# Kernel optimization log

Measured on AMD Instinct MI355X. Metric: run time of the kernel, lower is better.

## Reference

```python
import jax, jax.numpy as jnp
import numpy as np

T, N, D, H, E = 12, 10000, 256, 512, 160000
NUM_CONVS = 2  # num_layers - 1


def setup_inputs() -> dict:
    key = jax.random.key(0)
    ks = jax.random.split(key, 12)
    s_in = 1.0 / np.sqrt(D)
    s_h = 1.0 / np.sqrt(H)
    return {
        "xs": jax.random.normal(ks[0], (T, N, D), dtype=jnp.float32),
        "edge_index": jax.random.randint(ks[1], (2, E), 0, N, dtype=jnp.int64),
        "edge_weight": jax.random.uniform(ks[2], (E,), dtype=jnp.float32),
        # GRUCell params (PyTorch layout: [3H, D], [3H, H], [3H], [3H])
        "W_ih": jax.random.normal(ks[3], (3 * H, D), dtype=jnp.float32) * s_in,
        "W_hh": jax.random.normal(ks[4], (3 * H, H), dtype=jnp.float32) * s_h,
        "b_ih": jax.random.normal(ks[5], (3 * H,), dtype=jnp.float32) * s_h,
        "b_hh": jax.random.normal(ks[6], (3 * H,), dtype=jnp.float32) * s_h,
        # stacked GCNConv params
        "conv_W": jax.random.normal(ks[7], (NUM_CONVS, H, H), dtype=jnp.float32) * s_h,
        "conv_b": jnp.zeros((NUM_CONVS, H), dtype=jnp.float32),
        # final Linear(hidden_dim, 1)
        "lin_W": jax.random.normal(ks[8], (H, 1), dtype=jnp.float32) * s_h,
        "lin_b": jnp.zeros((1,), dtype=jnp.float32),
    }


def gru_cell(x, h, W_ih, W_hh, b_ih, b_hh):
    gi = x @ W_ih.T + b_ih  # (N, 3H)
    gh = h @ W_hh.T + b_hh  # (N, 3H)
    i_r, i_z, i_n = jnp.split(gi, 3, axis=-1)
    h_r, h_z, h_n = jnp.split(gh, 3, axis=-1)
    r = jax.nn.sigmoid(i_r + h_r)
    z = jax.nn.sigmoid(i_z + h_z)
    n = jnp.tanh(i_n + r * h_n)
    return (1.0 - z) * n + z * h


def reference(xs, edge_index, edge_weight, W_ih, W_hh, b_ih, b_hh,
              conv_W, conv_b, lin_W, lin_b):
    row, col = edge_index[0], edge_index[1]
    # GCN symmetric normalization with self-loops (PyG GCNConv default)
    deg = jax.ops.segment_sum(edge_weight, col, num_segments=N) + 1.0
    dinv = jax.lax.rsqrt(deg)
    norm = dinv[row] * edge_weight * dinv[col]  # (E,)
    self_w = dinv * dinv                        # (N,) self-loop coefficient

    def gcn(h, W, b):
        hW = h @ W  # (N, H)
        msg = norm[:, None] * hW[row]           # gather + weight
        agg = jax.ops.segment_sum(msg, col, num_segments=N)  # scatter-add
        return agg + self_w[:, None] * hW + b

    def step(h, x):
        h = gru_cell(x, h, W_ih, W_hh, b_ih, b_hh)
        for l in range(NUM_CONVS):
            h = jax.nn.relu(gcn(h, conv_W[l], conv_b[l]))
        # dropout is identity in eval mode
        out = h @ lin_W + lin_b  # (N, 1)
        return h, out

    h0 = jnp.zeros((N, H), dtype=xs.dtype)
    _, outs = jax.lax.scan(step, h0, xs)
    return outs  # (T, N, 1)
```

## Files before the change

kernel.cpp:

```cpp
#include <hip/hip_runtime.h>
#include <math.h>

#define T_STEPS 12
#define N_NODES 10000
#define MP 10112
#define D_IN 256
#define H_DIM 512
#define H3 1536
#define E_EDGES 160000
#define NUM_CONVS 2

typedef _Float16 f16x8 __attribute__((ext_vector_type(8)));
typedef float floatx4 __attribute__((ext_vector_type(4)));
typedef _Float16 f16x4 __attribute__((ext_vector_type(4)));
typedef unsigned short u16;
typedef unsigned int u32;

__device__ __forceinline__ float sigmoid_f(float x) {
  return __builtin_amdgcn_rcpf(1.0f + __expf(-x));
}
__device__ __forceinline__ float tanh_f(float x) {
  return 1.0f - 2.0f * __builtin_amdgcn_rcpf(1.0f + __expf(2.0f * x));
}

__device__ __forceinline__ void glds16(const void* g, void* l) {
  __builtin_amdgcn_global_load_lds(
      (const __attribute__((address_space(1))) unsigned int*)g,
      (__attribute__((address_space(3))) unsigned int*)l, 16, 0, 0);
}

#define MFMA16H(a, b, c) __builtin_amdgcn_mfma_f32_16x16x32_f16((a), (b), (c), 0, 0, 0)

__global__ __launch_bounds__(256) void gru_fused(
    const _Float16* __restrict__ X16,
    const _Float16* __restrict__ S16,
    const _Float16* __restrict__ Wih,
    const _Float16* __restrict__ Whh,
    const float* __restrict__ bihg, const float* __restrict__ bhhg,
    _Float16* __restrict__ G16) {
  __shared__ _Float16 As[4096];
  __shared__ _Float16 Bs[3072];
  const int tid = threadIdx.x;
  const int lane = tid & 63;
  const int wave = tid >> 6;
  const int bid = blockIdx.y * 16 + blockIdx.x;
  const int lid = (bid & 7) * 158 + (bid >> 3);
  const int bx = lid & 15, by = lid >> 4;
  const int rbase = by * 128;
  const int cbase = bx * 96;

  const int sa1 = tid, sa2 = tid + 256;
  const int ra1 = sa1 >> 2, ca1 = (sa1 & 3) ^ ((ra1 >> 1) & 3);
  const int ra2 = sa2 >> 2, ca2 = (sa2 & 3) ^ ((ra2 >> 1) & 3);
  const int la1 = (sa1 >> 6) << 9;
  const int la2 = (sa2 >> 6) << 9;
  const int sb1 = tid;
  const int rb1 = sb1 >> 2, cb1 = (sb1 & 3) ^ ((rb1 >> 1) & 3);
  const int lb1 = (sb1 >> 6) << 9;
  const int sb2 = 256 + tid;
  const int rb2 = sb2 >> 2, cb2 = (sb2 & 3) ^ ((rb2 >> 1) & 3);
  const int lb2 = (sb2 >> 6) << 9;

  const int wr = (wave >> 1) * 64;
  const int wc = (wave & 1) * 48;
  const int lrow = lane & 15;
  const int kq = lane >> 4;
  const int swz = kq ^ ((lrow >> 1) & 3);
  const int aoff = (wr + lrow) * 32 + swz * 8;
  const int boff = (wc + lrow) * 32 + swz * 8;

  floatx4 acc[4][4];
#pragma unroll
  for (int i = 0; i < 4; ++i)
#pragma unroll
    for (int g = 0; g < 4; ++g) acc[i][g] = (floatx4){0.f, 0.f, 0.f, 0.f};

  {
    const _Float16* pa1 = X16 + (size_t)(rbase + ra1) * 256 + ca1 * 8;
    const _Float16* pa2 = X16 + (size_t)(rbase + ra2) * 256 + ca2 * 8;
    const _Float16* pb1 = Wih + (size_t)(cbase + rb1) * 256 + cb1 * 8;
    const _Float16* pb2 = Wih + (size_t)(cbase + rb2) * 256 + cb2 * 8;
    for (int kt = 0; kt < 256; kt += 32) {
      glds16(pa1 + kt, &As[la1]);
      glds16(pa2 + kt, &As[la2]);
      glds16(pb1 + kt, &Bs[lb1]);
      if (tid < 128) glds16(pb2 + kt, &Bs[lb2]);
      __syncthreads();
      f16x8 ah[4], bh[3];
#pragma unroll
      for (int i = 0; i < 4; ++i) ah[i] = *(const f16x8*)&As[aoff + i * 512];
#pragma unroll
      for (int g = 0; g < 3; ++g) bh[g] = *(const f16x8*)&Bs[boff + g * 512];
#pragma unroll
      for (int i = 0; i < 4; ++i) {
        acc[i][0] = MFMA16H(ah[i], bh[0], acc[i][0]);
        acc[i][1] = MFMA16H(ah[i], bh[1], acc[i][1]);
        acc[i][2] = MFMA16H(ah[i], bh[2], acc[i][2]);
      }
      __syncthreads();
    }
  }
  {
    const _Float16* pa1 = S16 + (size_t)(rbase + ra1) * 512 + ca1 * 8;
    const _Float16* pa2 = S16 + (size_t)(rbase + ra2) * 512 + ca2 * 8;
    const _Float16* pb1 = Whh + (size_t)(cbase + rb1) * 512 + cb1 * 8;
    const _Float16* pb2 = Whh + (size_t)(cbase + rb2) * 512 + cb2 * 8;
    for (int kt = 0; kt < 512; kt += 32) {
      glds16(pa1 + kt, &As[la1]);
      glds16(pa2 + kt, &As[la2]);
      glds16(pb1 + kt, &Bs[lb1]);
      if (tid < 128) glds16(pb2 + kt, &Bs[lb2]);
      __syncthreads();
      f16x8 ah[4], bh[3];
#pragma unroll
      for (int i = 0; i < 4; ++i) ah[i] = *(const f16x8*)&As[aoff + i * 512];
#pragma unroll
      for (int g = 0; g < 3; ++g) bh[g] = *(const f16x8*)&Bs[boff + g * 512];
#pragma unroll
      for (int i = 0; i < 4; ++i) {
        acc[i][0] = MFMA16H(ah[i], bh[0], acc[i][0]);
        acc[i][1] = MFMA16H(ah[i], bh[1], acc[i][1]);
        acc[i][3] = MFMA16H(ah[i], bh[2], acc[i][3]);
      }
      __syncthreads();
    }
  }

  const int c0g = cbase + wc + lrow;
  const int j = (((bx << 1) | (wave & 1)) << 4) | lrow;
  const float brz0 = bihg[c0g] + bhhg[c0g];
  const float brz1 = bihg[c0g + 16] + bhhg[c0g + 16];
  const float bin = bihg[c0g + 32];
  const float bhn = bhhg[c0g + 32];
#pragma unroll
  for (int i = 0; i < 4; ++i) {
    int r0 = rbase + wr + i * 16 + kq * 4;
#pragma unroll
    for (int rr = 0; rr < 4; ++rr) {
      int row = r0 + rr;
      if (row >= N_NODES) continue;
      float r = sigmoid_f(acc[i][0][rr] + brz0);
      float z = sigmoid_f(acc[i][1][rr] + brz1);
      float nn = tanh_f(acc[i][2][rr] + bin + r * (acc[i][3][rr] + bhn));
      size_t o = (size_t)row * H_DIM + j;
      float hp = (float)S16[o];
      float hv = (1.0f - z) * nn + z * hp;
      G16[o] = (_Float16)hv;
    }
  }
}

__global__ __launch_bounds__(256) void gemm_conv(
    const u16* __restrict__ A16, const u16* __restrict__ B16,
    _Float16* __restrict__ C, int M, int Nn, int K) {
  __shared__ u16 As[2][2048];
  __shared__ u16 Bs[2][4096];
  const int tid = threadIdx.x;
  const int lane = tid & 63;
  const int wave = tid >> 6;
  const int bid = blockIdx.y * 4 + blockIdx.x;
  const int lid = (bid & 7) * 79 + (bid >> 3);
  const int bx = lid & 3, by = lid >> 2;
  const int rbase = by * 64;
  const int cbase = bx * 128;

  const int sa = tid;
  const int ra = sa >> 2, ca = (sa & 3) ^ ((ra >> 1) & 3);
  const int la = (sa >> 6) << 9;
  const int sb1 = tid, sb2 = tid + 256;
  const int rb1 = sb1 >> 2, cb1 = (sb1 & 3) ^ ((rb1 >> 1) & 3);
  const int rb2 = sb2 >> 2, cb2 = (sb2 & 3) ^ ((rb2 >> 1) & 3);
  const int lb1 = (sb1 >> 6) << 9, lb2 = (sb2 >> 6) << 9;
  const size_t oA = (size_t)(rbase + ra) * K + ca * 8;
  const size_t oB1 = (size_t)(cbase + rb1) * K + cb1 * 8;
  const size_t oB2 = (size_t)(cbase + rb2) * K + cb2 * 8;

  const int wr = (wave >> 1) * 32;
  const int wc = (wave & 1) * 64;
  const int lrow = lane & 15;
  const int kq = lane >> 4;
  const int swz = kq ^ ((lrow >> 1) & 3);
  const int aoff = (wr + lrow) * 32 + swz * 8;
  const int boff = (wc + lrow) * 32 + swz * 8;

  auto stage = [&](int buf, int t) {
    const int kt = t * 32;
    glds16(A16 + oA + kt, &As[buf][la]);
    glds16(B16 + oB1 + kt, &Bs[buf][lb1]);
    glds16(B16 + oB2 + kt, &Bs[buf][lb2]);
  };

  floatx4 acc[2][4];
#pragma unroll
  for (int i = 0; i < 2; ++i)
#pragma unroll
    for (int jj = 0; jj < 4; ++jj) acc[i][jj] = (floatx4){0.f, 0.f, 0.f, 0.f};

  const int NT = K >> 5;
  stage(0, 0);
  stage(1, 1);
  int cur = 0;
  for (int t = 0; t < NT; ++t) {
    if (t < NT - 1) asm volatile("s_waitcnt vmcnt(3)" ::: "memory");
    else            asm volatile("s_waitcnt vmcnt(0)" ::: "memory");
    __builtin_amdgcn_s_barrier();
    __builtin_amdgcn_sched_barrier(0);
    {
      f16x8 ah[2], bh[4];
#pragma unroll
      for (int i = 0; i < 2; ++i) ah[i] = *(const f16x8*)&As[cur][aoff + i * 512];
#pragma unroll
      for (int jj = 0; jj < 4; ++jj) bh[jj] = *(const f16x8*)&Bs[cur][boff + jj * 512];
      __builtin_amdgcn_s_setprio(1);
#pragma unroll
      for (int i = 0; i < 2; ++i)
#pragma unroll
        for (int jj = 0; jj < 4; ++jj) acc[i][jj] = MFMA16H(ah[i], bh[jj], acc[i][jj]);
      __builtin_amdgcn_s_setprio(0);
      __builtin_amdgcn_s_barrier();
    }
    __builtin_amdgcn_sched_barrier(0);
    if (t + 2 < NT) stage(cur, t + 2);
    cur ^= 1;
  }

#pragma unroll
  for (int jj = 0; jj < 4; ++jj) {
    int col = cbase + wc + jj * 16 + lrow;
#pragma unroll
    for (int i = 0; i < 2; ++i) {
      int r0 = rbase + wr + i * 16 + kq * 4;
#pragma unroll
      for (int rr = 0; rr < 4; ++rr) {
        int row = r0 + rr;
        if (row < M) C[(size_t)row * Nn + col] = (_Float16)acc[i][jj][rr];
      }
    }
  }
}

__global__ void split_grouped16(const float* __restrict__ W, _Float16* __restrict__ w16,
                                int K) {
  int i = blockIdx.x * 256 + threadIdx.x;
  if (i >= H3 * K) return;
  int r3h = i / K, k = i - r3h * K;
  int g = r3h >> 9, j = r3h & 511;
  int nr = ((j >> 4) * 48) + (g << 4) + (j & 15);
  w16[(size_t)nr * K + k] = (_Float16)W[i];
}

__global__ void bias_grouped(const float* __restrict__ bih, const float* __restrict__ bhh,
                             float* __restrict__ bihg, float* __restrict__ bhhg) {
  int n = blockIdx.x * 256 + threadIdx.x;
  if (n >= H3) return;
  int g = n >> 9, j = n & 511;
  int nr = ((j >> 4) * 48) + (g << 4) + (j & 15);
  bihg[nr] = bih[n];
  bhhg[nr] = bhh[n];
}

__global__ void split_convw(const float* __restrict__ W, _Float16* __restrict__ w16) {
  int o = blockIdx.x * 256 + threadIdx.x;
  if (o >= NUM_CONVS * H_DIM * H_DIM) return;
  int k = o & 511, j = (o >> 9) & 511, l = o >> 18;
  float v = W[(size_t)l * H_DIM * H_DIM + (size_t)k * H_DIM + j];
  w16[o] = (_Float16)v;
}

__global__ void split_xs16(const float* __restrict__ xs, _Float16* __restrict__ x16) {
  const int QP = MP * D_IN / 4;
  int q = blockIdx.x * 256 + threadIdx.x;
  if (q >= T_STEPS * QP) return;
  int t = q / QP;
  int rem = (q - t * QP) * 4;
  size_t o = (size_t)t * MP * D_IN + rem;
  f16x4 v16 = {(_Float16)0.f, (_Float16)0.f, (_Float16)0.f, (_Float16)0.f};
  if (rem < N_NODES * D_IN) {
    float4 v = *(const float4*)(xs + (size_t)t * N_NODES * D_IN + rem);
    v16[0] = (_Float16)v.x;
    v16[1] = (_Float16)v.y;
    v16[2] = (_Float16)v.z;
    v16[3] = (_Float16)v.w;
  }
  *(f16x4*)(x16 + o) = v16;
}

__global__ void deg_kernel(const int* __restrict__ col, const float* __restrict__ w,
                           float* __restrict__ deg, int* __restrict__ counts) {
  int e = blockIdx.x * blockDim.x + threadIdx.x;
  if (e >= E_EDGES) return;
  int c = col[e];
  atomicAdd(&deg[c], w[e]);
  atomicAdd(&counts[c], 1);
}

__global__ void dinv_kernel(float* __restrict__ deg_dinv, float* __restrict__ selfw) {
  int n = blockIdx.x * blockDim.x + threadIdx.x;
  if (n >= N_NODES) return;
  float d = deg_dinv[n] + 1.0f;
  float di = 1.0f / sqrtf(d);
  deg_dinv[n] = di;
  selfw[n] = 1.0f / d;
}

__global__ __launch_bounds__(1024) void scan_kernel(const int* __restrict__ counts,
                                                    int* __restrict__ offsets, int n) {
  __shared__ int smem[1024];
  __shared__ int carry_s;
  if (threadIdx.x == 0) carry_s = 0;
  __syncthreads();
  for (int base = 0; base < n; base += 1024) {
    int i = base + threadIdx.x;
    int v = (i < n) ? counts[i] : 0;
    smem[threadIdx.x] = v;
    __syncthreads();
    for (int off = 1; off < 1024; off <<= 1) {
      int t = (threadIdx.x >= off) ? smem[threadIdx.x - off] : 0;
      __syncthreads();
      smem[threadIdx.x] += t;
      __syncthreads();
    }
    if (i < n) offsets[i] = carry_s + smem[threadIdx.x] - v;
    int total = smem[1023];
    __syncthreads();
    if (threadIdx.x == 0) carry_s += total;
    __syncthreads();
  }
  if (threadIdx.x == 0) offsets[n] = carry_s;
}

__global__ void scatter_kernel(const int* __restrict__ row, const int* __restrict__ col,
                               const float* __restrict__ w, const float* __restrict__ dinv,
                               const int* __restrict__ offsets, int* __restrict__ cursor,
                               int* __restrict__ csr_row, float* __restrict__ csr_norm) {
  int e = blockIdx.x * blockDim.x + threadIdx.x;
  if (e >= E_EDGES) return;
  int r = row[e], c = col[e];
  float nrm = dinv[r] * w[e] * dinv[c];
  int pos = offsets[c] + atomicAdd(&cursor[c], 1);
  csr_row[pos] = r;
  csr_norm[pos] = nrm;
}

__device__ __forceinline__ void fma8h(float* a, float w, const _Float16* p) {
  f16x4 x = *(const f16x4*)p;
  f16x4 y = *(const f16x4*)(p + 256);
  a[0] = fmaf(w, (float)x[0], a[0]);
  a[1] = fmaf(w, (float)x[1], a[1]);
  a[2] = fmaf(w, (float)x[2], a[2]);
  a[3] = fmaf(w, (float)x[3], a[3]);
  a[4] = fmaf(w, (float)y[0], a[4]);
  a[5] = fmaf(w, (float)y[1], a[5]);
  a[6] = fmaf(w, (float)y[2], a[6]);
  a[7] = fmaf(w, (float)y[3], a[7]);
}

template <bool FINAL>
__global__ __launch_bounds__(256) void agg_kernel(
    const _Float16* __restrict__ hW, const int* __restrict__ csr_row,
    const float* __restrict__ csr_norm, const int* __restrict__ offsets,
    const float* __restrict__ selfw, const float* __restrict__ bias,
    _Float16* __restrict__ dst,
    const float* __restrict__ lw, const float* __restrict__ lb,
    float* __restrict__ out) {
  const int n = (blockIdx.x << 2) | (threadIdx.x >> 6);
  const int lane = threadIdx.x & 63;
  if (n >= N_NODES) return;
  const int c0 = lane << 2;
  const int beg = offsets[n], end = offsets[n + 1];
  float a0[8] = {}, a1[8] = {};
  int j = beg;
  for (; j + 4 <= end; j += 4) {
    int r0 = csr_row[j], r1 = csr_row[j + 1], r2 = csr_row[j + 2], r3 = csr_row[j + 3];
    float w0 = csr_norm[j], w1 = csr_norm[j + 1], w2 = csr_norm[j + 2], w3 = csr_norm[j + 3];
    fma8h(a0, w0, hW + (size_t)r0 * H_DIM + c0);
    fma8h(a1, w1, hW + (size_t)r1 * H_DIM + c0);
    fma8h(a0, w2, hW + (size_t)r2 * H_DIM + c0);
    fma8h(a1, w3, hW + (size_t)r3 * H_DIM + c0);
  }
  for (; j < end; ++j) fma8h(a0, csr_norm[j], hW + (size_t)csr_row[j] * H_DIM + c0);

  const float sw = selfw[n];
  const _Float16* ps = hW + (size_t)n * H_DIM + c0;
  f16x4 sa = *(const f16x4*)ps;
  f16x4 sb = *(const f16x4*)(ps + 256);
  float4 ba = *(const float4*)(bias + c0);
  float4 bb = *(const float4*)(bias + 256 + c0);
  float v[8];
  v[0] = fmaxf(fmaf(sw, (float)sa[0], a0[0] + a1[0]) + ba.x, 0.f);
  v[1] = fmaxf(fmaf(sw, (float)sa[1], a0[1] + a1[1]) + ba.y, 0.f);
  v[2] = fmaxf(fmaf(sw, (float)sa[2], a0[2] + a1[2]) + ba.z, 0.f);
  v[3] = fmaxf(fmaf(sw, (float)sa[3], a0[3] + a1[3]) + ba.w, 0.f);
  v[4] = fmaxf(fmaf(sw, (float)sb[0], a0[4] + a1[4]) + bb.x, 0.f);
  v[5] = fmaxf(fmaf(sw, (float)sb[1], a0[5] + a1[5]) + bb.y, 0.f);
  v[6] = fmaxf(fmaf(sw, (float)sb[2], a0[6] + a1[6]) + bb.z, 0.f);
  v[7] = fmaxf(fmaf(sw, (float)sb[3], a0[7] + a1[7]) + bb.w, 0.f);

  size_t o = (size_t)n * H_DIM + c0;
  f16x4 ga = {(_Float16)v[0], (_Float16)v[1], (_Float16)v[2], (_Float16)v[3]};
  f16x4 gb = {(_Float16)v[4], (_Float16)v[5], (_Float16)v[6], (_Float16)v[7]};
  *(f16x4*)(dst + o) = ga;
  *(f16x4*)(dst + o + 256) = gb;

  if (FINAL) {
    float4 la = *(const float4*)(lw + c0);
    float4 lbv = *(const float4*)(lw + 256 + c0);
    float s = v[0] * la.x + v[1] * la.y + v[2] * la.z + v[3] * la.w +
              v[4] * lbv.x + v[5] * lbv.y + v[6] * lbv.z + v[7] * lbv.w;
#pragma unroll
    for (int off2 = 32; off2 > 0; off2 >>= 1) s += __shfl_down(s, off2, 64);
    if (lane == 0) out[n] = s + lb[0];
  }
}

extern "C" void kernel_launch(void* const* d_in, const int* in_sizes, int n_in,
                              void* d_out, int out_size, void* d_ws, size_t ws_size,
                              hipStream_t stream) {
  const float* xs = (const float*)d_in[0];
  const int* ei = (const int*)d_in[1];
  const float* ew = (const float*)d_in[2];
  const float* W_ih = (const float*)d_in[3];
  const float* W_hh = (const float*)d_in[4];
  const float* b_ih = (const float*)d_in[5];
  const float* b_hh = (const float*)d_in[6];
  const float* conv_W = (const float*)d_in[7];
  const float* conv_b = (const float*)d_in[8];
  const float* lin_W = (const float*)d_in[9];
  const float* lin_b = (const float*)d_in[10];
  float* out = (float*)d_out;

  const int* row = ei;
  const int* col = ei + E_EDGES;

  char* ws = (char*)d_ws;
  size_t off = 0;
  auto alloc = [&](size_t bytes) -> void* {
    void* p = ws + off;
    off += (bytes + 255) & ~(size_t)255;
    return p;
  };
  _Float16* S16 = (_Float16*)alloc((size_t)MP * H_DIM * 2);
  _Float16* G16 = (_Float16*)alloc((size_t)MP * H_DIM * 2);
  _Float16* hW16 = (_Float16*)alloc((size_t)MP * H_DIM * 2);
  _Float16* xs16 = (_Float16*)alloc((size_t)T_STEPS * MP * D_IN * 2);
  _Float16* Wih16 = (_Float16*)alloc((size_t)H3 * D_IN * 2);
  _Float16* Whh16 = (_Float16*)alloc((size_t)H3 * H_DIM * 2);
  _Float16* Wc16 = (_Float16*)alloc((size_t)NUM_CONVS * H_DIM * H_DIM * 2);
  float* bihg = (float*)alloc(H3 * 4);
  float* bhhg = (float*)alloc(H3 * 4);
  float* dinv = (float*)alloc(N_NODES * 4);
  float* selfw = (float*)alloc(N_NODES * 4);
  float* csr_norm = (float*)alloc(E_EDGES * 4);
  int* csr_row = (int*)alloc(E_EDGES * 4);
  int* offsets = (int*)alloc((N_NODES + 1) * 4);
  int* counts = (int*)alloc(N_NODES * 4);
  int* cursor = (int*)alloc(N_NODES * 4);

  hipMemsetAsync(S16, 0, (size_t)MP * H_DIM * 2, stream);
  hipMemsetAsync(G16, 0, (size_t)MP * H_DIM * 2, stream);
  hipMemsetAsync(hW16, 0, (size_t)MP * H_DIM * 2, stream);
  hipMemsetAsync(dinv, 0, N_NODES * 4, stream);
  hipMemsetAsync(counts, 0, N_NODES * 4, stream);
  hipMemsetAsync(cursor, 0, N_NODES * 4, stream);

  deg_kernel<<<(E_EDGES + 255) / 256, 256, 0, stream>>>(col, ew, dinv, counts);
  dinv_kernel<<<(N_NODES + 255) / 256, 256, 0, stream>>>(dinv, selfw);
  scan_kernel<<<1, 1024, 0, stream>>>(counts, offsets, N_NODES);
  scatter_kernel<<<(E_EDGES + 255) / 256, 256, 0, stream>>>(row, col, ew, dinv, offsets,
                                                            cursor, csr_row, csr_norm);
  split_grouped16<<<(H3 * D_IN + 255) / 256, 256, 0, stream>>>(W_ih, Wih16, D_IN);
  split_grouped16<<<(H3 * H_DIM + 255) / 256, 256, 0, stream>>>(W_hh, Whh16, H_DIM);
  bias_grouped<<<(H3 + 255) / 256, 256, 0, stream>>>(b_ih, b_hh, bihg, bhhg);
  split_convw<<<(NUM_CONVS * H_DIM * H_DIM + 255) / 256, 256, 0, stream>>>(conv_W, Wc16);
  split_xs16<<<(T_STEPS * MP * D_IN / 4 + 255) / 256, 256, 0, stream>>>(xs, xs16);

  dim3 blk(256);
  dim3 g_gru(16, MP / 128);
  dim3 g_conv(H_DIM / 128, MP / 64);
  int g_agg = (N_NODES + 3) / 4;

  for (int t = 0; t < T_STEPS; ++t) {
    gru_fused<<<g_gru, blk, 0, stream>>>(
        xs16 + (size_t)t * MP * D_IN, S16, Wih16, Whh16, bihg, bhhg, G16);
    gemm_conv<<<g_conv, blk, 0, stream>>>((const u16*)G16, (const u16*)Wc16, hW16,
                                          N_NODES, H_DIM, H_DIM);
    agg_kernel<false><<<g_agg, 256, 0, stream>>>(
        hW16, csr_row, csr_norm, offsets, selfw, conv_b, G16,
        nullptr, nullptr, nullptr);
    gemm_conv<<<g_conv, blk, 0, stream>>>(
        (const u16*)G16, (const u16*)(Wc16 + (size_t)H_DIM * H_DIM), hW16,
        N_NODES, H_DIM, H_DIM);
    agg_kernel<true><<<g_agg, 256, 0, stream>>>(
        hW16, csr_row, csr_norm, offsets, selfw, conv_b + H_DIM, S16,
        lin_W, lin_b, out + (size_t)t * N_NODES);
  }
}
```

Measured before the change: 1.652 ms.

## Double-buffer GRU GEMM LDS tiles with async prefetch and vmcnt waits

Converts the fused GRU GEMM main loop from single-buffered LDS staging with two syncthreads per k-step into a double-buffered pipeline. The x and hidden-state phases are merged into one 24-step loop that prefetches two stages ahead, waiting with per-wave vmcnt counts (waves 0-1 issue four loads per stage, waves 2-3 three) and raw s_barrier calls. It also raises wave priority around the MFMA bursts. The goal is to hide global-to-LDS load latency behind matrix math, at the cost of doubled LDS use and fragile hand-counted waitcnt logic.

```diff
diff --git a/kernel.cpp b/kernel.cpp
--- a/kernel.cpp
+++ b/kernel.cpp
@@ -31,6 +31,27 @@
 
 #define MFMA16H(a, b, c) __builtin_amdgcn_mfma_f32_16x16x32_f16((a), (b), (c), 0, 0, 0)
 
+template <int G2>
+__device__ __forceinline__ void gru_kstep(const _Float16 (&As)[2][4096],
+                                          const _Float16 (&Bs)[2][3072], int cur,
+                                          int aoff, int boff,
+                                          floatx4 (&acc)[4][4]) {
+  f16x8 ah[4], bh[3];
+#pragma unroll
+  for (int i = 0; i < 4; ++i) ah[i] = *(const f16x8*)&As[cur][aoff + i * 512];
+#pragma unroll
+  for (int g = 0; g < 3; ++g) bh[g] = *(const f16x8*)&Bs[cur][boff + g * 512];
+  __builtin_amdgcn_s_setprio(1);
+#pragma unroll
+  for (int i = 0; i < 4; ++i) {
+    acc[i][0] = MFMA16H(ah[i], bh[0], acc[i][0]);
+    acc[i][1] = MFMA16H(ah[i], bh[1], acc[i][1]);
+    acc[i][G2] = MFMA16H(ah[i], bh[2], acc[i][G2]);
+  }
+  __builtin_amdgcn_s_setprio(0);
+  __builtin_amdgcn_s_barrier();
+}
+
 __global__ __launch_bounds__(256) void gru_fused(
     const _Float16* __restrict__ X16,
     const _Float16* __restrict__ S16,
@@ -38,8 +59,8 @@
     const _Float16* __restrict__ Whh,
     const float* __restrict__ bihg, const float* __restrict__ bhhg,
     _Float16* __restrict__ G16) {
-  __shared__ _Float16 As[4096];
-  __shared__ _Float16 Bs[3072];
+  __shared__ _Float16 As[2][4096];
+  __shared__ _Float16 Bs[2][3072];
   const int tid = threadIdx.x;
   const int lane = tid & 63;
   const int wave = tid >> 6;
@@ -69,61 +90,63 @@
   const int aoff = (wr + lrow) * 32 + swz * 8;
   const int boff = (wc + lrow) * 32 + swz * 8;
 
+  const size_t xA1 = (size_t)(rbase + ra1) * 256 + ca1 * 8;
+  const size_t xA2 = (size_t)(rbase + ra2) * 256 + ca2 * 8;
+  const size_t hA1 = (size_t)(rbase + ra1) * 512 + ca1 * 8;
+  const size_t hA2 = (size_t)(rbase + ra2) * 512 + ca2 * 8;
+  const size_t xB1 = (size_t)(cbase + rb1) * 256 + cb1 * 8;
+  const size_t xB2 = (size_t)(cbase + rb2) * 256 + cb2 * 8;
+  const size_t hB1 = (size_t)(cbase + rb1) * 512 + cb1 * 8;
+  const size_t hB2 = (size_t)(cbase + rb2) * 512 + cb2 * 8;
+
+  auto stage = [&](int buf, int t) {
+    if (t < 8) {
+      const int kt = t * 32;
+      glds16(X16 + xA1 + kt, &As[buf][la1]);
+      glds16(X16 + xA2 + kt, &As[buf][la2]);
+      glds16(Wih + xB1 + kt, &Bs[buf][lb1]);
+      if (tid < 128) glds16(Wih + xB2 + kt, &Bs[buf][lb2]);
+    } else {
+      const int kt = (t - 8) * 32;
+      glds16(S16 + hA1 + kt, &As[buf][la1]);
+      glds16(S16 + hA2 + kt, &As[buf][la2]);
+      glds16(Whh + hB1 + kt, &Bs[buf][lb1]);
+      if (tid < 128) glds16(Whh + hB2 + kt, &Bs[buf][lb2]);
+    }
+  };
+
   floatx4 acc[4][4];
 #pragma unroll
   for (int i = 0; i < 4; ++i)
 #pragma unroll
     for (int g = 0; g < 4; ++g) acc[i][g] = (floatx4){0.f, 0.f, 0.f, 0.f};
 
-  {
-    const _Float16* pa1 = X16 + (size_t)(rbase + ra1) * 256 + ca1 * 8;
-    const _Float16* pa2 = X16 + (size_t)(rbase + ra2) * 256 + ca2 * 8;
-    const _Float16* pb1 = Wih + (size_t)(cbase + rb1) * 256 + cb1 * 8;
-    const _Float16* pb2 = Wih + (size_t)(cbase + rb2) * 256 + cb2 * 8;
-    for (int kt = 0; kt < 256; kt += 32) {
-      glds16(pa1 + kt, &As[la1]);
-      glds16(pa2 + kt, &As[la2]);
-      glds16(pb1 + kt, &Bs[lb1]);
-      if (tid < 128) glds16(pb2 + kt, &Bs[lb2]);
-      __syncthreads();
-      f16x8 ah[4], bh[3];
-#pragma unroll
-      for (int i = 0; i < 4; ++i) ah[i] = *(const f16x8*)&As[aoff + i * 512];
-#pragma unroll
-      for (int g = 0; g < 3; ++g) bh[g] = *(const f16x8*)&Bs[boff + g * 512];
-#pragma unroll
-      for (int i = 0; i < 4; ++i) {
-        acc[i][0] = MFMA16H(ah[i], bh[0], acc[i][0]);
-        acc[i][1] = MFMA16H(ah[i], bh[1], acc[i][1]);
-        acc[i][2] = MFMA16H(ah[i], bh[2], acc[i][2]);
-      }
-      __syncthreads();
+  stage(0, 0);
+  stage(1, 1);
+  int cur = 0;
+  for (int t = 0; t < 8; ++t) {
+    if (wave < 2) asm volatile("s_waitcnt vmcnt(4)" ::: "memory");
+    else          asm volatile("s_waitcnt vmcnt(3)" ::: "memory");
+    __builtin_amdgcn_s_barrier();
+    __builtin_amdgcn_sched_barrier(0);
+    gru_kstep<2>(As, Bs, cur, aoff, boff, acc);
+    __builtin_amdgcn_sched_barrier(0);
+    stage(cur, t + 2);
+    cur ^= 1;
+  }
+  for (int t = 8; t < 24; ++t) {
+    if (t < 23) {
+      if (wave < 2) asm volatile("s_waitcnt vmcnt(4)" ::: "memory");
+      else          asm volatile("s_waitcnt vmcnt(3)" ::: "memory");
+    } else {
+      asm volatile("s_waitcnt vmcnt(0)" ::: "memory");
     }
-  }
-  {
-    const _Float16* pa1 = S16 + (size_t)(rbase + ra1) * 512 + ca1 * 8;
-    const _Float16* pa2 = S16 + (size_t)(rbase + ra2) * 512 + ca2 * 8;
-    const _Float16* pb1 = Whh + (size_t)(cbase + rb1) * 512 + cb1 * 8;
-    const _Float16* pb2 = Whh + (size_t)(cbase + rb2) * 512 + cb2 * 8;
-    for (int kt = 0; kt < 512; kt += 32) {
-      glds16(pa1 + kt, &As[la1]);
-      glds16(pa2 + kt, &As[la2]);
-      glds16(pb1 + kt, &Bs[lb1]);
-      if (tid < 128) glds16(pb2 + kt, &Bs[lb2]);
-      __syncthreads();
-      f16x8 ah[4], bh[3];
-#pragma unroll
-      for (int i = 0; i < 4; ++i) ah[i] = *(const f16x8*)&As[aoff + i * 512];
-#pragma unroll
-      for (int g = 0; g < 3; ++g) bh[g] = *(const f16x8*)&Bs[boff + g * 512];
-#pragma unroll
-      for (int i = 0; i < 4; ++i) {
-        acc[i][0] = MFMA16H(ah[i], bh[0], acc[i][0]);
-        acc[i][1] = MFMA16H(ah[i], bh[1], acc[i][1]);
-        acc[i][3] = MFMA16H(ah[i], bh[2], acc[i][3]);
-      }
-      __syncthreads();
-    }
+    __builtin_amdgcn_s_barrier();
+    __builtin_amdgcn_sched_barrier(0);
+    gru_kstep<3>(As, Bs, cur, aoff, boff, acc);
+    __builtin_amdgcn_sched_barrier(0);
+    if (t + 2 < 24) stage(cur, t + 2);
+    cur ^= 1;
   }
 
   const int c0g = cbase + wc + lrow;
```

New measurement: 1.621 ms. Within noise of the previous version (-1.9%).
